# Optimization experiments

Hardware: AMD Instinct MI355X
Metric: run time of the kernel (lower is better)

## Reference

```python
import jax, jax.numpy as jnp
import numpy as np

B, UNITS, DIM = 8192, 2048, 32


def setup_inputs() -> dict:
    key = jax.random.key(0)
    kx, kc = jax.random.split(key)
    x = jax.random.normal(kx, (B, DIM), dtype=jnp.float32)
    # centers initialized with RandomUniform(0, 1) as in the keras layer
    centers = jax.random.uniform(kc, (UNITS, DIM), dtype=jnp.float32)
    gamma = jnp.ones((1,), dtype=jnp.float32)  # Constant(1.0), non-trainable
    return {"x": x, "centers": centers, "gamma": gamma}


def reference(x, centers, gamma):
    # diff: [B, units, dim] broadcasted, then sum of squares over dim -> [B, units]
    diff = x[:, None, :] - centers[None, :, :]
    sq_dist = jnp.sum(diff * diff, axis=-1)
    return jnp.exp(-gamma * sq_dist)  # gamma shape (1,) broadcasts
```

## Files before the change

kernel.cpp:

```cpp
#include <hip/hip_runtime.h>
#include <math.h>


#define BATCH   8192
#define UNITS   2048
#define DIM     32
#define BM      64
#define BN      128
#define THREADS 256
#define NXCD    8
#define ITERS   4

typedef __attribute__((ext_vector_type(8))) short s16x8;
typedef __attribute__((ext_vector_type(4))) float f32x4;

static __device__ __forceinline__ unsigned bf16_rne(float v) {
    unsigned u = __builtin_bit_cast(unsigned, v);
    return (u + 0x7FFFu + ((u >> 16) & 1u)) >> 16;
}

static __device__ __forceinline__ void load8(const float* __restrict__ p, float* v) {
    float4 t0 = *reinterpret_cast<const float4*>(p);
    float4 t1 = *reinterpret_cast<const float4*>(p + 4);
    v[0] = t0.x; v[1] = t0.y; v[2] = t0.z; v[3] = t0.w;
    v[4] = t1.x; v[5] = t1.y; v[6] = t1.z; v[7] = t1.w;
}

static __device__ __forceinline__ void split8(const float* v, s16x8& hi, s16x8& lo) {
#pragma unroll
    for (int j = 0; j < 8; ++j) {
        unsigned h = bf16_rne(v[j]);
        float hf = __builtin_bit_cast(float, h << 16);
        unsigned l = bf16_rne(v[j] - hf);
        hi[j] = (short)h;
        lo[j] = (short)l;
    }
}

__global__ __launch_bounds__(THREADS) void rbf_stream(
    const float* __restrict__ x,
    const float* __restrict__ centers,
    const float* __restrict__ gamma,
    float* __restrict__ out)
{
    const int tid  = threadIdx.x;
    const int wid  = tid >> 6;
    const int lane = tid & 63;
    const int wm   = wid >> 1;
    const int wn   = wid & 1;
    const int l16  = lane & 15;
    const int kq   = lane >> 4;

    const int bid = blockIdx.x;
    const int xcd = bid & (NXCD - 1);
    const int rlo = bid >> 3;
    const int cb  = rlo & 15;
    const int sb  = rlo >> 4;
    const int c0  = cb * BN;

    const float kg = -gamma[0] * 1.4426950408889634f;
    const float m2 = -2.0f * kg;

    s16x8 b_hi[4], b_lo[4];
    float kgcnq[4][4];
#pragma unroll
    for (int n = 0; n < 4; ++n) {
        float v[8];
        load8(centers + (size_t)(c0 + wn * 64 + n * 16 + l16) * DIM + kq * 8, v);
        split8(v, b_hi[n], b_lo[n]);
        float pn = 0.f;
#pragma unroll
        for (int j = 0; j < 8; ++j) pn = fmaf(v[j], v[j], pn);
        pn += __shfl_xor(pn, 16);
        pn += __shfl_xor(pn, 32);
#pragma unroll
        for (int j = 0; j < 4; ++j)
            kgcnq[n][j] = kg * __shfl(pn, kq * 4 + j);
    }

    float xf[2][2][8];
    {
        const int r0 = (xcd * 16 + sb) * BM;
#pragma unroll
        for (int m = 0; m < 2; ++m)
            load8(x + (size_t)(r0 + wm * 32 + m * 16 + l16) * DIM + kq * 8, xf[0][m]);
    }

#pragma unroll
    for (int k = 0; k < ITERS; ++k) {
        const int cur = k & 1;
        const int r0  = (xcd * 16 + k * 4 + sb) * BM;

        if (k + 1 < ITERS) {
            const int r1 = (xcd * 16 + (k + 1) * 4 + sb) * BM;
#pragma unroll
            for (int m = 0; m < 2; ++m)
                load8(x + (size_t)(r1 + wm * 32 + m * 16 + l16) * DIM + kq * 8,
                      xf[cur ^ 1][m]);
        }

        s16x8 a_hi[2], a_lo[2];
        float kgxn[2];
#pragma unroll
        for (int m = 0; m < 2; ++m) {
            split8(xf[cur][m], a_hi[m], a_lo[m]);
            float pn = 0.f;
#pragma unroll
            for (int j = 0; j < 8; ++j) pn = fmaf(xf[cur][m][j], xf[cur][m][j], pn);
            pn += __shfl_xor(pn, 16);
            pn += __shfl_xor(pn, 32);
            kgxn[m] = kg * pn;
        }

#pragma unroll
        for (int m = 0; m < 2; ++m) {
#pragma unroll
            for (int n = 0; n < 4; ++n) {
                f32x4 acc = {0.f, 0.f, 0.f, 0.f};
                acc = __builtin_amdgcn_mfma_f32_16x16x32_bf16(b_lo[n], a_hi[m], acc, 0, 0, 0);
                acc = __builtin_amdgcn_mfma_f32_16x16x32_bf16(b_hi[n], a_lo[m], acc, 0, 0, 0);
                acc = __builtin_amdgcn_mfma_f32_16x16x32_bf16(b_hi[n], a_hi[m], acc, 0, 0, 0);

                float4 o;
                o.x = __builtin_amdgcn_exp2f(fmaf(m2, acc[0], kgxn[m] + kgcnq[n][0]));
                o.y = __builtin_amdgcn_exp2f(fmaf(m2, acc[1], kgxn[m] + kgcnq[n][1]));
                o.z = __builtin_amdgcn_exp2f(fmaf(m2, acc[2], kgxn[m] + kgcnq[n][2]));
                o.w = __builtin_amdgcn_exp2f(fmaf(m2, acc[3], kgxn[m] + kgcnq[n][3]));

                float* op = out + (size_t)(r0 + wm * 32 + m * 16 + l16) * UNITS
                                + (c0 + wn * 64 + n * 16 + kq * 4);
                *reinterpret_cast<float4*>(op) = o;
            }
        }
    }
}

extern "C" void kernel_launch(void* const* d_in, const int* in_sizes, int n_in,
                              void* d_out, int out_size, void* d_ws, size_t ws_size,
                              hipStream_t stream)
{
    const float* x       = (const float*)d_in[0];
    const float* centers = (const float*)d_in[1];
    const float* gamma   = (const float*)d_in[2];
    float* out           = (float*)d_out;

    dim3 grid(512);
    dim3 block(THREADS);
    rbf_stream<<<grid, block, 0, stream>>>(x, centers, gamma, out);
}
```

Baseline: 20.41 us.

## Stage output tiles through LDS for full-row coalesced stores, one wave per row strip

Each wave now computes a 16x128 output strip instead of a 32x64 quadrant, holding all eight center fragments in registers. Results are written to a swizzled per-wave LDS buffer and then read back so each store instruction writes contiguous 512-byte row segments. This targets write-bandwidth inefficiency from scattered 64-byte partial-row stores. It costs 32 KB LDS per block, extra LDS traffic, and higher register use for the doubled center fragments, with launch bounds set for two blocks per CU.

Result: slower. 22.15 us (+8.5%).

```diff
diff --git a/kernel.cpp b/kernel.cpp
--- a/kernel.cpp
+++ b/kernel.cpp
@@ -37,17 +37,17 @@
     }
 }
 
-__global__ __launch_bounds__(THREADS) void rbf_stream(
+__global__ __launch_bounds__(THREADS, 2) void rbf_stream(
     const float* __restrict__ x,
     const float* __restrict__ centers,
     const float* __restrict__ gamma,
     float* __restrict__ out)
 {
+    __shared__ __align__(16) f32x4 s_t[4][16][32];
+
     const int tid  = threadIdx.x;
-    const int wid  = tid >> 6;
+    const int w    = tid >> 6;
     const int lane = tid & 63;
-    const int wm   = wid >> 1;
-    const int wn   = wid & 1;
     const int l16  = lane & 15;
     const int kq   = lane >> 4;
 
@@ -61,12 +61,12 @@
     const float kg = -gamma[0] * 1.4426950408889634f;
     const float m2 = -2.0f * kg;
 
-    s16x8 b_hi[4], b_lo[4];
-    float kgcnq[4][4];
+    s16x8 b_hi[8], b_lo[8];
+    float kgcnq[8][4];
 #pragma unroll
-    for (int n = 0; n < 4; ++n) {
+    for (int n = 0; n < 8; ++n) {
         float v[8];
-        load8(centers + (size_t)(c0 + wn * 64 + n * 16 + l16) * DIM + kq * 8, v);
+        load8(centers + (size_t)(c0 + n * 16 + l16) * DIM + kq * 8, v);
         split8(v, b_hi[n], b_lo[n]);
         float pn = 0.f;
 #pragma unroll
@@ -78,13 +78,8 @@
             kgcnq[n][j] = kg * __shfl(pn, kq * 4 + j);
     }
 
-    float xf[2][2][8];
-    {
-        const int r0 = (xcd * 16 + sb) * BM;
-#pragma unroll
-        for (int m = 0; m < 2; ++m)
-            load8(x + (size_t)(r0 + wm * 32 + m * 16 + l16) * DIM + kq * 8, xf[0][m]);
-    }
+    float xf[2][8];
+    load8(x + (size_t)((xcd * 16 + sb) * BM + w * 16 + l16) * DIM + kq * 8, xf[0]);
 
 #pragma unroll
     for (int k = 0; k < ITERS; ++k) {
@@ -93,44 +88,43 @@
 
         if (k + 1 < ITERS) {
             const int r1 = (xcd * 16 + (k + 1) * 4 + sb) * BM;
-#pragma unroll
-            for (int m = 0; m < 2; ++m)
-                load8(x + (size_t)(r1 + wm * 32 + m * 16 + l16) * DIM + kq * 8,
-                      xf[cur ^ 1][m]);
+            load8(x + (size_t)(r1 + w * 16 + l16) * DIM + kq * 8, xf[cur ^ 1]);
         }
 
-        s16x8 a_hi[2], a_lo[2];
-        float kgxn[2];
+        s16x8 a_hi, a_lo;
+        split8(xf[cur], a_hi, a_lo);
+        float pn = 0.f;
 #pragma unroll
-        for (int m = 0; m < 2; ++m) {
-            split8(xf[cur][m], a_hi[m], a_lo[m]);
-            float pn = 0.f;
+        for (int j = 0; j < 8; ++j) pn = fmaf(xf[cur][j], xf[cur][j], pn);
+        pn += __shfl_xor(pn, 16);
+        pn += __shfl_xor(pn, 32);
+        const float kgxn = kg * pn;
+
 #pragma unroll
-            for (int j = 0; j < 8; ++j) pn = fmaf(xf[cur][m][j], xf[cur][m][j], pn);
-            pn += __shfl_xor(pn, 16);
-            pn += __shfl_xor(pn, 32);
-            kgxn[m] = kg * pn;
+        for (int n = 0; n < 8; ++n) {
+            f32x4 acc = {0.f, 0.f, 0.f, 0.f};
+            acc = __builtin_amdgcn_mfma_f32_16x16x32_bf16(b_lo[n], a_hi, acc, 0, 0, 0);
+            acc = __builtin_amdgcn_mfma_f32_16x16x32_bf16(b_hi[n], a_lo, acc, 0, 0, 0);
+            acc = __builtin_amdgcn_mfma_f32_16x16x32_bf16(b_hi[n], a_hi, acc, 0, 0, 0);
+
+            f32x4 o;
+            o[0] = __builtin_amdgcn_exp2f(fmaf(m2, acc[0], kgxn + kgcnq[n][0]));
+            o[1] = __builtin_amdgcn_exp2f(fmaf(m2, acc[1], kgxn + kgcnq[n][1]));
+            o[2] = __builtin_amdgcn_exp2f(fmaf(m2, acc[2], kgxn + kgcnq[n][2]));
+            o[3] = __builtin_amdgcn_exp2f(fmaf(m2, acc[3], kgxn + kgcnq[n][3]));
+
+            const int s = ((n * 4 + kq) + l16 * 4) & 31;
+            s_t[w][l16][s] = o;
         }
 
 #pragma unroll
-        for (int m = 0; m < 2; ++m) {
-#pragma unroll
-            for (int n = 0; n < 4; ++n) {
-                f32x4 acc = {0.f, 0.f, 0.f, 0.f};
-                acc = __builtin_amdgcn_mfma_f32_16x16x32_bf16(b_lo[n], a_hi[m], acc, 0, 0, 0);
-                acc = __builtin_amdgcn_mfma_f32_16x16x32_bf16(b_hi[n], a_lo[m], acc, 0, 0, 0);
-                acc = __builtin_amdgcn_mfma_f32_16x16x32_bf16(b_hi[n], a_hi[m], acc, 0, 0, 0);
-
-                float4 o;
-                o.x = __builtin_amdgcn_exp2f(fmaf(m2, acc[0], kgxn[m] + kgcnq[n][0]));
-                o.y = __builtin_amdgcn_exp2f(fmaf(m2, acc[1], kgxn[m] + kgcnq[n][1]));
-                o.z = __builtin_amdgcn_exp2f(fmaf(m2, acc[2], kgxn[m] + kgcnq[n][2]));
-                o.w = __builtin_amdgcn_exp2f(fmaf(m2, acc[3], kgxn[m] + kgcnq[n][3]));
-
-                float* op = out + (size_t)(r0 + wm * 32 + m * 16 + l16) * UNITS
-                                + (c0 + wn * 64 + n * 16 + kq * 4);
-                *reinterpret_cast<float4*>(op) = o;
-            }
+        for (int p = 0; p < 8; ++p) {
+            const int row = 2 * p + (lane >> 5);
+            const int sl  = ((lane & 31) + row * 4) & 31;
+            f32x4 v = s_t[w][row][sl];
+            float* op = out + (size_t)(r0 + w * 16 + row) * UNITS
+                            + c0 + (lane & 31) * 4;
+            *reinterpret_cast<f32x4*>(op) = v;
         }
     }
 }
```
